# Optimization experiments

Hardware: AMD Instinct MI355X
Metric: run time of the kernel (lower is better)

## Reference

```python
import jax, jax.numpy as jnp
import numpy as np

N_NODES = 100000
N_EDGES = 1600000
IN_C = 64
HID = 64
OUT_C = 40


def setup_inputs() -> dict:
    key = jax.random.key(0)
    ks = jax.random.split(key, 12)
    def lin_init(k, fan_in, shape):
        bound = 1.0 / np.sqrt(fan_in)
        return jax.random.uniform(k, shape, jnp.float32, -bound, bound)
    x0 = jax.random.normal(ks[0], (N_NODES, IN_C), jnp.float32)
    edge_index = jax.random.randint(ks[1], (2, N_EDGES), 0, N_NODES, jnp.int64)
    return {
        "x0": x0,
        "edge_index": edge_index,
        "W1": lin_init(ks[2], IN_C, (HID, IN_C)),
        "b1": lin_init(ks[3], IN_C, (HID,)),
        "Wr1": lin_init(ks[4], IN_C, (HID, IN_C)),
        "br1": lin_init(ks[5], IN_C, (HID,)),
        "W2": lin_init(ks[6], HID, (HID, HID)),
        "b2": lin_init(ks[7], HID, (HID,)),
        "Wr2": lin_init(ks[8], HID, (HID, HID)),
        "br2": lin_init(ks[9], HID, (HID,)),
        "Wl": lin_init(ks[10], 2 * HID, (OUT_C, 2 * HID)),
        "bl": lin_init(ks[11], 2 * HID, (OUT_C,)),
    }


def _norm_weights(row, col, num_nodes):
    # symmetric degree normalization: d^-1/2[row] * d^-1/2[col]
    ones = jnp.ones(row.shape[0], jnp.float32)
    deg = jax.ops.segment_sum(ones, row, num_segments=num_nodes)
    dis = jnp.where(deg > 0, jax.lax.rsqrt(jnp.maximum(deg, 1.0)) * jnp.where(deg > 0, 1.0, 0.0), 0.0)
    dis = jnp.where(deg > 0, deg ** -0.5, 0.0)
    return dis[row] * dis[col]


def _bigraph_conv(x, row, col, w, W, b, Wr, br, num_nodes):
    h = x @ W.T + b                                    # [N, out]
    msg = w[:, None] * h[col]                          # gather + scale, [E, out]
    agg = jax.ops.segment_sum(msg, row, num_segments=num_nodes)
    return agg + x @ Wr.T + br


def reference(x0, edge_index, W1, b1, Wr1, br1, W2, b2, Wr2, br2, Wl, bl):
    num_nodes = x0.shape[0]
    row, col = edge_index[0], edge_index[1]
    w = _norm_weights(row, col, num_nodes)
    x1 = jax.nn.relu(_bigraph_conv(x0, row, col, w, W1, b1, Wr1, br1, num_nodes))
    x2 = jax.nn.relu(_bigraph_conv(x1, row, col, w, W2, b2, Wr2, br2, num_nodes))
    x = jnp.concatenate([x1, x2], axis=-1)
    logits = x @ Wl.T + bl
    return jax.nn.log_softmax(logits, axis=-1)
```

## Files before the change

kernel.cpp:

```cpp
#include <hip/hip_runtime.h>
#include <math.h>


typedef unsigned short u16;
typedef unsigned int   u32;

#define BROWS 512
#define BIN_CHUNK 8192
#define CAPB 12288

__device__ __forceinline__ u16 f2bf(float f) {
  u32 u = __float_as_uint(f);
  u32 r = u + 0x7fffu + ((u >> 16) & 1u);
  return (u16)(r >> 16);
}
__device__ __forceinline__ float bf2f(u16 h) {
  return __uint_as_float(((u32)h) << 16);
}

__global__ __launch_bounds__(1024) void k_binA(
    const int* __restrict__ row, const int* __restrict__ col,
    unsigned* __restrict__ bCnt, unsigned* __restrict__ pairs,
    int nE, int NB, int capA)
{
  __shared__ unsigned buf[BIN_CHUNK];
  __shared__ unsigned cnt[16][256];
  __shared__ unsigned base[256], gb[256], tot[256], sc[256];
  const int t = threadIdx.x;
  const int wave = t >> 6, lane = t & 63;
  const int tb = blockIdx.x * BIN_CHUNK;

  for (int i = t; i < 16 * 256; i += 1024) ((unsigned*)cnt)[i] = 0;
  __syncthreads();

  unsigned pk[8];
  unsigned short po[8];
  short bk[8];
#pragma unroll
  for (int j = 0; j < 8; ++j) {
    int i = tb + j * 1024 + t;
    if (i < nE) {
      int r = row[i], c = col[i];
      int b = r >> 9;
      pk[j] = ((unsigned)(r & (BROWS - 1)) << 17) | (unsigned)c;
      bk[j] = (short)b;
      po[j] = (unsigned short)atomicAdd(&cnt[wave][b], 1u);
    } else bk[j] = -1;
  }
  __syncthreads();

  if (t < 256) {
    unsigned run = 0;
#pragma unroll
    for (int w = 0; w < 16; ++w) {
      unsigned c = cnt[w][t];
      cnt[w][t] = run;
      run += c;
    }
    tot[t] = run;
    sc[t] = run;
  }
  __syncthreads();
  for (int off = 1; off < 256; off <<= 1) {
    unsigned v = 0;
    if (t < 256 && t >= off) v = sc[t - off];
    __syncthreads();
    if (t < 256) sc[t] += v;
    __syncthreads();
  }
  if (t < 256) {
    base[t] = t ? sc[t - 1] : 0u;
    unsigned c = tot[t];
    gb[t] = c ? atomicAdd(&bCnt[t], c) : 0u;
  }
  __syncthreads();

#pragma unroll
  for (int j = 0; j < 8; ++j)
    if (bk[j] >= 0) buf[base[bk[j]] + cnt[wave][bk[j]] + po[j]] = pk[j];
  __syncthreads();

  for (int b = wave; b < NB; b += 16) {
    unsigned cb = tot[b];
    if (!cb) continue;
    unsigned lo = base[b], g = gb[b];
    size_t dst = (size_t)b * (unsigned)capA;
    for (unsigned u = lane; u < cb; u += 64)
      if (g + u < (unsigned)capA) pairs[dst + g + u] = buf[lo + u];
  }
}

__global__ __launch_bounds__(256) void k_bscan(const unsigned* __restrict__ bCnt,
                                               unsigned* __restrict__ bBase, int NB) {
  __shared__ unsigned sc[256];
  int t = threadIdx.x;
  unsigned v = (t < NB) ? min(bCnt[t], (unsigned)CAPB) : 0u;
  sc[t] = v;
  __syncthreads();
  for (int off = 1; off < 256; off <<= 1) {
    unsigned u = (t >= off) ? sc[t - off] : 0u;
    __syncthreads();
    sc[t] += u;
    __syncthreads();
  }
  if (t < NB) bBase[t] = t ? sc[t - 1] : 0u;
}

__global__ __launch_bounds__(512) void k_binB(
    const unsigned* __restrict__ pairs, const unsigned* __restrict__ bCnt,
    const unsigned* __restrict__ bBase, int* __restrict__ colS,
    unsigned* __restrict__ start, float* __restrict__ dis,
    int N, int capA)
{
  __shared__ unsigned hist[BROWS], ex[BROWS], cur[BROWS], sc[BROWS];
  __shared__ unsigned cols[CAPB];
  const int t = threadIdx.x;
  const int b = blockIdx.x;
  const unsigned cnt = min(bCnt[b], (unsigned)CAPB);
  const unsigned gbase = bBase[b];
  const size_t src = (size_t)b * (unsigned)capA;

  hist[t] = 0;
  __syncthreads();
  for (unsigned i = t; i < cnt; i += 512)
    atomicAdd(&hist[pairs[src + i] >> 17], 1u);
  __syncthreads();
  const unsigned h = hist[t];
  sc[t] = h;
  __syncthreads();
  for (int off = 1; off < 512; off <<= 1) {
    unsigned v = (t >= off) ? sc[t - off] : 0u;
    __syncthreads();
    sc[t] += v;
    __syncthreads();
  }
  const unsigned e = sc[t] - h;
  ex[t] = e; cur[t] = e;
  __syncthreads();
  for (unsigned i = t; i < cnt; i += 512) {
    unsigned p = pairs[src + i];
    unsigned pos = atomicAdd(&cur[p >> 17], 1u);
    cols[pos] = p & 0x1FFFFu;
  }
  __syncthreads();
  for (unsigned i = t; i < cnt; i += 512)
    colS[gbase + i] = (int)cols[i];
  const int n = b * BROWS + t;
  if (n < N) {
    start[n] = gbase + e + h;
    dis[n] = h ? rsqrtf((float)h) : 0.f;
  }
}

__global__ __launch_bounds__(256) void k_deg(const int* __restrict__ row,
                                             unsigned* __restrict__ deg, int nE) {
  int i = blockIdx.x * blockDim.x + threadIdx.x;
  int stride = gridDim.x * blockDim.x;
  for (; i < nE; i += stride) atomicAdd(&deg[row[i]], 1u);
}

__global__ __launch_bounds__(256) void k_dis(const unsigned* __restrict__ deg,
                                             float* __restrict__ dis, int n) {
  int i = blockIdx.x * blockDim.x + threadIdx.x;
  if (i < n) {
    unsigned d = deg[i];
    dis[i] = d > 0u ? rsqrtf((float)d) : 0.f;
  }
}

__global__ __launch_bounds__(256) void k_scan1(const unsigned* __restrict__ deg,
                                               unsigned* __restrict__ start,
                                               unsigned* __restrict__ bsum, int n) {
  __shared__ unsigned s[256];
  const int base = blockIdx.x * 2048;
  unsigned v[8], tsum = 0;
#pragma unroll
  for (int j = 0; j < 8; ++j) {
    int idx = base + threadIdx.x * 8 + j;
    v[j] = idx < n ? deg[idx] : 0u;
    tsum += v[j];
  }
  s[threadIdx.x] = tsum;
  __syncthreads();
  for (int off = 1; off < 256; off <<= 1) {
    unsigned t = (threadIdx.x >= off) ? s[threadIdx.x - off] : 0u;
    __syncthreads();
    s[threadIdx.x] += t;
    __syncthreads();
  }
  unsigned run = threadIdx.x ? s[threadIdx.x - 1] : 0u;
  if (threadIdx.x == 255) bsum[blockIdx.x] = s[255];
#pragma unroll
  for (int j = 0; j < 8; ++j) {
    int idx = base + threadIdx.x * 8 + j;
    if (idx < n) start[idx] = run;
    run += v[j];
  }
}

__global__ void k_scan2(unsigned* __restrict__ bsum, int nB) {
  if (threadIdx.x == 0 && blockIdx.x == 0) {
    unsigned run = 0;
    for (int b = 0; b < nB; ++b) { unsigned t = bsum[b]; bsum[b] = run; run += t; }
  }
}

__global__ __launch_bounds__(256) void k_scan3(unsigned* __restrict__ start,
                                               const unsigned* __restrict__ bsum, int n) {
  int i = blockIdx.x * blockDim.x + threadIdx.x;
  if (i < n) start[i] += bsum[i >> 11];
}

__global__ __launch_bounds__(256) void k_build(const int* __restrict__ row,
                                               const int* __restrict__ col,
                                               unsigned* __restrict__ start,
                                               int* __restrict__ colS, int nE) {
  int i = blockIdx.x * blockDim.x + threadIdx.x;
  int stride = gridDim.x * blockDim.x;
  for (; i < nE; i += stride) {
    int r = row[i];
    unsigned p = atomicAdd(&start[r], 1u);
    colS[p] = col[i];
  }
}

__global__ __launch_bounds__(256) void k_cast(const float4* __restrict__ x4,
                                              ushort4* __restrict__ out, int n4) {
  int i = blockIdx.x * blockDim.x + threadIdx.x;
  int stride = gridDim.x * blockDim.x;
  for (; i < n4; i += stride) {
    float4 f = x4[i];
    ushort4 v;
    v.x = f2bf(f.x); v.y = f2bf(f.y); v.z = f2bf(f.z); v.w = f2bf(f.w);
    out[i] = v;
  }
}

__global__ __launch_bounds__(256) void k_prep(
    const float* __restrict__ W1, const float* __restrict__ b1,
    const float* __restrict__ Wr1, const float* __restrict__ br1,
    const float* __restrict__ W2, const float* __restrict__ b2,
    const float* __restrict__ Wr2, const float* __restrict__ br2,
    float4* __restrict__ UT)
{
  int i = blockIdx.x * 256 + threadIdx.x;
  if (i >= 2 * 33 * 64) return;
  int layer = i / (33 * 64);
  int kq = (i / 64) % 33;
  int o = i % 64;
  const float* W  = layer ? W2  : W1;
  const float* Wr = layer ? Wr2 : Wr1;
  const float* b  = layer ? b2  : b1;
  const float* br = layer ? br2 : br1;
  float4 v;
  if (kq < 16)       v = ((const float4*)W)[o * 16 + kq];
  else if (kq < 32)  v = ((const float4*)Wr)[o * 16 + kq - 16];
  else               v = make_float4(b[o], br[o], 0.f, 0.f);
  UT[i] = v;
}

__global__ __launch_bounds__(256) void k_spmm_h(
    const u16* __restrict__ xh, u16* __restrict__ aggh, float* __restrict__ rs,
    const int* __restrict__ colS, const unsigned* __restrict__ startEnd,
    const float* __restrict__ dis, int nNodes)
{
  const int t = threadIdx.x, wave = t >> 6, lane = t & 63;
  const int g = lane >> 4, sub = lane & 15;
  const int n = blockIdx.x * 4 + wave;
  if (n >= nNodes) return;
  const unsigned lo = n ? startEnd[n - 1] : 0u;
  const unsigned hi = startEnd[n];
  const ushort4* h4 = (const ushort4*)xh;
  float ax = 0.f, ay = 0.f, az = 0.f, aw = 0.f, sw = 0.f;
  for (unsigned base = lo; base < hi; base += 64) {
    const int cnt = (int)min(64u, hi - base);
    int   myc = (lane < cnt) ? colS[base + lane] : 0;
    float myw = (lane < cnt) ? dis[myc] : 0.f;
    sw += myw;
    for (int j = 0; j < cnt; j += 16) {
      int ja = j + g, jb = j + 4 + g, jc = j + 8 + g, jd = j + 12 + g;
      int   c0 = __shfl(myc, ja); float w0 = __shfl(myw, ja);
      int   c1 = __shfl(myc, jb); float w1 = __shfl(myw, jb);
      int   c2 = __shfl(myc, jc); float w2 = __shfl(myw, jc);
      int   c3 = __shfl(myc, jd); float w3 = __shfl(myw, jd);
      ushort4 v0 = h4[(size_t)c0 * 16 + sub];
      ushort4 v1 = h4[(size_t)c1 * 16 + sub];
      ushort4 v2 = h4[(size_t)c2 * 16 + sub];
      ushort4 v3 = h4[(size_t)c3 * 16 + sub];
      ax += w0 * bf2f(v0.x) + w1 * bf2f(v1.x) + w2 * bf2f(v2.x) + w3 * bf2f(v3.x);
      ay += w0 * bf2f(v0.y) + w1 * bf2f(v1.y) + w2 * bf2f(v2.y) + w3 * bf2f(v3.y);
      az += w0 * bf2f(v0.z) + w1 * bf2f(v1.z) + w2 * bf2f(v2.z) + w3 * bf2f(v3.z);
      aw += w0 * bf2f(v0.w) + w1 * bf2f(v1.w) + w2 * bf2f(v2.w) + w3 * bf2f(v3.w);
    }
  }
  ax += __shfl_xor(ax, 16); ay += __shfl_xor(ay, 16);
  az += __shfl_xor(az, 16); aw += __shfl_xor(aw, 16);
  ax += __shfl_xor(ax, 32); ay += __shfl_xor(ay, 32);
  az += __shfl_xor(az, 32); aw += __shfl_xor(aw, 32);
  sw += __shfl_xor(sw, 1);  sw += __shfl_xor(sw, 2);
  sw += __shfl_xor(sw, 4);  sw += __shfl_xor(sw, 8);
  sw += __shfl_xor(sw, 16); sw += __shfl_xor(sw, 32);
  const float dn = dis[n];
  if (lane < 16) {
    ushort4 o;
    o.x = f2bf(dn * ax); o.y = f2bf(dn * ay);
    o.z = f2bf(dn * az); o.w = f2bf(dn * aw);
    ((ushort4*)aggh)[(size_t)n * 16 + sub] = o;
  }
  if (lane == 0) rs[n] = dn * sw;
}

__global__ __launch_bounds__(256) void k_gemv(
    const u16* __restrict__ aggh, const float* __restrict__ rs,
    const u16* __restrict__ rooth, const float4* __restrict__ UT,
    u16* __restrict__ xo, int nNodes)
{
  __shared__ u16 xsh[64][136];
  const int t = threadIdx.x;
  const int lane = t & 63;
  const int og = __builtin_amdgcn_readfirstlane(t >> 6);
  const int n0 = blockIdx.x * 64;

  {
    const int r = t >> 2, q = t & 3;
    int gn = n0 + r; if (gn > nNodes - 1) gn = nNodes - 1;
    const uint4* a = (const uint4*)(aggh + (size_t)gn * 64);
    const uint4* x = (const uint4*)(rooth + (size_t)gn * 64);
    *(uint4*)&xsh[r][q * 16]           = a[q * 2];
    *(uint4*)&xsh[r][q * 16 + 8]       = a[q * 2 + 1];
    *(uint4*)&xsh[r][64 + q * 16]      = x[q * 2];
    *(uint4*)&xsh[r][64 + q * 16 + 8]  = x[q * 2 + 1];
  }
  __syncthreads();

  float acc[16];
#pragma unroll
  for (int j = 0; j < 16; ++j) acc[j] = 0.f;

#pragma unroll 4
  for (int k = 0; k < 32; ++k) {
    ushort4 v = *(const ushort4*)&xsh[lane][k * 4];
    float xa = bf2f(v.x), xb = bf2f(v.y), xc = bf2f(v.z), xd = bf2f(v.w);
    const float4* w = UT + k * 64 + og * 16;
#pragma unroll
    for (int j = 0; j < 16; ++j) {
      float4 W = w[j];
      acc[j] = fmaf(xa, W.x, fmaf(xb, W.y, fmaf(xc, W.z, fmaf(xd, W.w, acc[j]))));
    }
  }

  const int n = n0 + lane;
  const float rsv = (n < nNodes) ? rs[n] : 0.f;
  {
    const float4* w = UT + 32 * 64 + og * 16;
#pragma unroll
    for (int j = 0; j < 16; ++j) {
      float4 W = w[j];
      acc[j] = fmaf(rsv, W.x, acc[j]) + W.y;
    }
  }

  if (n < nNodes) {
    uint4 u0, u1;
    u0.x = (u32)f2bf(fmaxf(acc[0], 0.f))  | ((u32)f2bf(fmaxf(acc[1], 0.f)) << 16);
    u0.y = (u32)f2bf(fmaxf(acc[2], 0.f))  | ((u32)f2bf(fmaxf(acc[3], 0.f)) << 16);
    u0.z = (u32)f2bf(fmaxf(acc[4], 0.f))  | ((u32)f2bf(fmaxf(acc[5], 0.f)) << 16);
    u0.w = (u32)f2bf(fmaxf(acc[6], 0.f))  | ((u32)f2bf(fmaxf(acc[7], 0.f)) << 16);
    u1.x = (u32)f2bf(fmaxf(acc[8], 0.f))  | ((u32)f2bf(fmaxf(acc[9], 0.f)) << 16);
    u1.y = (u32)f2bf(fmaxf(acc[10], 0.f)) | ((u32)f2bf(fmaxf(acc[11], 0.f)) << 16);
    u1.z = (u32)f2bf(fmaxf(acc[12], 0.f)) | ((u32)f2bf(fmaxf(acc[13], 0.f)) << 16);
    u1.w = (u32)f2bf(fmaxf(acc[14], 0.f)) | ((u32)f2bf(fmaxf(acc[15], 0.f)) << 16);
    uint4* dst = (uint4*)(xo + (size_t)n * 64 + og * 16);
    dst[0] = u0;
    dst[1] = u1;
  }
}

__global__ __launch_bounds__(256) void k_final(
    const u16* __restrict__ x1h, const u16* __restrict__ x2h,
    const float* __restrict__ Wl, const float* __restrict__ bl,
    float* __restrict__ out, int nNodes)
{
  __shared__ float4 xs[64][33];
  __shared__ float redM[64][4];
  __shared__ float redS[64][4];
  const int t = threadIdx.x;
  const int lane = t & 63;
  const int og = __builtin_amdgcn_readfirstlane(t >> 6);
  const int nodeBase = blockIdx.x * 64;

  {
    const int sn = t >> 2, q = t & 3;
    int gn = nodeBase + sn;
    if (gn > nNodes - 1) gn = nNodes - 1;
    const ushort4* a = (q < 2) ? (const ushort4*)(x1h + (size_t)gn * 64)
                               : (const ushort4*)(x2h + (size_t)gn * 64);
    const int qq = q & 1;
#pragma unroll
    for (int j = 0; j < 8; ++j) {
      ushort4 v = a[qq * 8 + j];
      xs[sn][q * 8 + j] = make_float4(bf2f(v.x), bf2f(v.y), bf2f(v.z), bf2f(v.w));
    }
  }
  __syncthreads();

  const float4* W4 = (const float4*)Wl;
  float acc[10];
#pragma unroll
  for (int j = 0; j < 10; ++j) acc[j] = bl[og * 10 + j];
  for (int k = 0; k < 32; ++k) {
    float4 x = xs[lane][k];
#pragma unroll
    for (int j = 0; j < 10; ++j) {
      float4 w = W4[(og * 10 + j) * 32 + k];
      acc[j] += w.x * x.x + w.y * x.y + w.z * x.z + w.w * x.w;
    }
  }

  float m10 = acc[0];
#pragma unroll
  for (int j = 1; j < 10; ++j) m10 = fmaxf(m10, acc[j]);
  redM[lane][og] = m10;
  __syncthreads();
  float M = fmaxf(fmaxf(redM[lane][0], redM[lane][1]),
                  fmaxf(redM[lane][2], redM[lane][3]));
  float s10 = 0.f;
#pragma unroll
  for (int j = 0; j < 10; ++j) s10 += __expf(acc[j] - M);
  redS[lane][og] = s10;
  __syncthreads();
  const float S = redS[lane][0] + redS[lane][1] + redS[lane][2] + redS[lane][3];
  const float lse = M + __logf(S);

  const int n = nodeBase + lane;
  if (n < nNodes) {
    float2* o2 = (float2*)(out + (size_t)n * 40 + og * 10);
#pragma unroll
    for (int q = 0; q < 5; ++q)
      o2[q] = make_float2(acc[2 * q] - lse, acc[2 * q + 1] - lse);
  }
}

extern "C" void kernel_launch(void* const* d_in, const int* in_sizes, int n_in,
                              void* d_out, int out_size, void* d_ws, size_t ws_size,
                              hipStream_t stream) {
  const float* x0  = (const float*)d_in[0];
  const int*   ei  = (const int*)d_in[1];
  const float* W1  = (const float*)d_in[2];
  const float* b1  = (const float*)d_in[3];
  const float* Wr1 = (const float*)d_in[4];
  const float* br1 = (const float*)d_in[5];
  const float* W2  = (const float*)d_in[6];
  const float* b2  = (const float*)d_in[7];
  const float* Wr2 = (const float*)d_in[8];
  const float* br2 = (const float*)d_in[9];
  const float* Wl  = (const float*)d_in[10];
  const float* bl  = (const float*)d_in[11];
  float* out = (float*)d_out;

  const int N = in_sizes[0] / 64;
  const int E = in_sizes[1] / 2;
  const int* row = ei;
  const int* col = ei + E;

  const int NB = (N + BROWS - 1) / BROWS;
  const int capA = 16384;
  const int avg = E / (NB > 0 ? NB : 1);
  const bool binOK = (N <= 131072) && (NB <= 256) &&
                     (avg + 12 * (int)sqrtf((float)avg + 1.f) + 256 <= CAPB);

  size_t P = (size_t)NB * capA;
  if (P < (size_t)32 * N) P = (size_t)32 * N;

  const size_t UT_W = 2 * 33 * 64 * 4;
  const size_t needBin = 4 * (512 + P + (size_t)E + (size_t)3 * N + UT_W +
                              (size_t)32 * N + (size_t)32 * N);
  const size_t needCSR = 4 * ((size_t)4 * N + 64 + (size_t)E + UT_W +
                              (size_t)32 * N + (size_t)32 * N + (size_t)32 * N);

  unsigned *start = nullptr; float *dis = nullptr, *rsv = nullptr;
  int* colS = nullptr; float4* UT = nullptr;
  u16 *aggh = nullptr, *x0h = nullptr, *x1h = nullptr, *x2h = nullptr;
  bool ok = false;

  if (binOK && ws_size >= needBin) {
    unsigned* bCnt  = (unsigned*)d_ws;
    unsigned* bBase = bCnt + 256;
    unsigned* pairs = bBase + 256;
    colS  = (int*)(pairs + P);
    start = (unsigned*)(colS + E);
    dis   = (float*)(start + N);
    rsv   = dis + N;
    UT    = (float4*)(rsv + N);
    aggh  = (u16*)(UT + 2 * 33 * 64);
    x1h   = aggh + (size_t)64 * N;
    x0h   = (u16*)pairs;
    x2h   = (u16*)pairs;

    hipMemsetAsync(bCnt, 0, 256 * 4, stream);
    k_binA<<<(E + BIN_CHUNK - 1) / BIN_CHUNK, 1024, 0, stream>>>(row, col, bCnt, pairs, E, NB, capA);
    k_bscan<<<1, 256, 0, stream>>>(bCnt, bBase, NB);
    k_binB<<<NB, 512, 0, stream>>>(pairs, bCnt, bBase, colS, start, dis, N, capA);
    ok = true;
  } else if (ws_size >= needCSR) {
    unsigned* deg = (unsigned*)d_ws;
    start = deg + N;
    dis   = (float*)(start + N);
    rsv   = dis + N;
    unsigned* bsum = (unsigned*)(rsv + N);
    colS  = (int*)(bsum + 64);
    UT    = (float4*)(colS + E);
    aggh  = (u16*)(UT + 2 * 33 * 64);
    x1h   = aggh + (size_t)64 * N;
    u16* xsh = x1h + (size_t)64 * N;
    x0h = xsh; x2h = xsh;

    const int nB = (N + 2047) / 2048;
    hipMemsetAsync(deg, 0, (size_t)N * 4, stream);
    k_deg<<<1024, 256, 0, stream>>>(row, deg, E);
    k_dis<<<(N + 255) / 256, 256, 0, stream>>>(deg, dis, N);
    k_scan1<<<nB, 256, 0, stream>>>(deg, start, bsum, N);
    k_scan2<<<1, 64, 0, stream>>>(bsum, nB);
    k_scan3<<<(N + 255) / 256, 256, 0, stream>>>(start, bsum, N);
    k_build<<<1024, 256, 0, stream>>>(row, col, start, colS, E);
    ok = true;
  }

  if (!ok) return;

  k_cast<<<1024, 256, 0, stream>>>((const float4*)x0, (ushort4*)x0h, N * 16);
  k_prep<<<17, 256, 0, stream>>>(W1, b1, Wr1, br1, W2, b2, Wr2, br2, UT);

  k_spmm_h<<<(N + 3) / 4, 256, 0, stream>>>(x0h, aggh, rsv, colS, start, dis, N);
  k_gemv<<<(N + 63) / 64, 256, 0, stream>>>(aggh, rsv, x0h, UT, x1h, N);

  k_spmm_h<<<(N + 3) / 4, 256, 0, stream>>>(x1h, aggh, rsv, colS, start, dis, N);
  k_gemv<<<(N + 63) / 64, 256, 0, stream>>>(aggh, rsv, x1h, UT + 33 * 64, x2h, N);

  k_final<<<(N + 63) / 64, 256, 0, stream>>>(x1h, x2h, Wl, bl, out, N);
}
```

Before: 225.0 us.

## Precompute packed column/weight records and map one node per 16 lanes in SpMM

Adds a pass that builds per-edge (column, dis[col]) records and the row weight sums once, so both SpMM layers read packed records instead of gathering dis per edge and recomputing sums. The SpMM kernel now assigns 16 lanes per node instead of a whole 64-lane wave, removing shuffles and idle lanes for low-degree nodes. It costs an extra kernel and 8 bytes per edge of extra workspace traffic. Each node's lanes read its records serially.

```diff
diff --git a/kernel.cpp b/kernel.cpp
--- a/kernel.cpp
+++ b/kernel.cpp
@@ -112,7 +112,7 @@
     unsigned* __restrict__ start, float* __restrict__ dis,
     int N, int capA)
 {
-  __shared__ unsigned hist[BROWS], ex[BROWS], cur[BROWS], sc[BROWS];
+  __shared__ unsigned hist[BROWS], cur[BROWS], sc[BROWS];
   __shared__ unsigned cols[CAPB];
   const int t = threadIdx.x;
   const int b = blockIdx.x;
@@ -135,7 +135,7 @@
     __syncthreads();
   }
   const unsigned e = sc[t] - h;
-  ex[t] = e; cur[t] = e;
+  cur[t] = e;
   __syncthreads();
   for (unsigned i = t; i < cnt; i += 512) {
     unsigned p = pairs[src + i];
@@ -222,6 +222,29 @@
     unsigned p = atomicAdd(&start[r], 1u);
     colS[p] = col[i];
   }
+}
+
+__global__ __launch_bounds__(256) void k_wgt(
+    const int* __restrict__ colS, const unsigned* __restrict__ startEnd,
+    const float* __restrict__ dis, uint2* __restrict__ rec,
+    float* __restrict__ rs, int nNodes)
+{
+  const int t = threadIdx.x;
+  const int sub = t & 15;
+  const int n = blockIdx.x * 16 + (t >> 4);
+  if (n >= nNodes) return;
+  const unsigned lo = n ? startEnd[n - 1] : 0u;
+  const unsigned hi = startEnd[n];
+  float s = 0.f;
+  for (unsigned u = lo + sub; u < hi; u += 16) {
+    int c = colS[u];
+    float w = dis[c];
+    rec[u] = make_uint2((unsigned)c, __float_as_uint(w));
+    s += w;
+  }
+  s += __shfl_xor(s, 1); s += __shfl_xor(s, 2);
+  s += __shfl_xor(s, 4); s += __shfl_xor(s, 8);
+  if (sub == 0) rs[n] = dis[n] * s;
 }
 
 __global__ __launch_bounds__(256) void k_cast(const float4* __restrict__ x4,
@@ -259,55 +282,47 @@
   UT[i] = v;
 }
 
-__global__ __launch_bounds__(256) void k_spmm_h(
-    const u16* __restrict__ xh, u16* __restrict__ aggh, float* __restrict__ rs,
-    const int* __restrict__ colS, const unsigned* __restrict__ startEnd,
+__global__ __launch_bounds__(256) void k_spmm_rec(
+    const u16* __restrict__ xh, u16* __restrict__ aggh,
+    const uint2* __restrict__ rec, const unsigned* __restrict__ startEnd,
     const float* __restrict__ dis, int nNodes)
 {
-  const int t = threadIdx.x, wave = t >> 6, lane = t & 63;
-  const int g = lane >> 4, sub = lane & 15;
-  const int n = blockIdx.x * 4 + wave;
+  const int t = threadIdx.x;
+  const int sub = t & 15;
+  const int n = blockIdx.x * 16 + (t >> 4);
   if (n >= nNodes) return;
   const unsigned lo = n ? startEnd[n - 1] : 0u;
   const unsigned hi = startEnd[n];
   const ushort4* h4 = (const ushort4*)xh;
-  float ax = 0.f, ay = 0.f, az = 0.f, aw = 0.f, sw = 0.f;
-  for (unsigned base = lo; base < hi; base += 64) {
-    const int cnt = (int)min(64u, hi - base);
-    int   myc = (lane < cnt) ? colS[base + lane] : 0;
-    float myw = (lane < cnt) ? dis[myc] : 0.f;
-    sw += myw;
-    for (int j = 0; j < cnt; j += 16) {
-      int ja = j + g, jb = j + 4 + g, jc = j + 8 + g, jd = j + 12 + g;
-      int   c0 = __shfl(myc, ja); float w0 = __shfl(myw, ja);
-      int   c1 = __shfl(myc, jb); float w1 = __shfl(myw, jb);
-      int   c2 = __shfl(myc, jc); float w2 = __shfl(myw, jc);
-      int   c3 = __shfl(myc, jd); float w3 = __shfl(myw, jd);
-      ushort4 v0 = h4[(size_t)c0 * 16 + sub];
-      ushort4 v1 = h4[(size_t)c1 * 16 + sub];
-      ushort4 v2 = h4[(size_t)c2 * 16 + sub];
-      ushort4 v3 = h4[(size_t)c3 * 16 + sub];
-      ax += w0 * bf2f(v0.x) + w1 * bf2f(v1.x) + w2 * bf2f(v2.x) + w3 * bf2f(v3.x);
-      ay += w0 * bf2f(v0.y) + w1 * bf2f(v1.y) + w2 * bf2f(v2.y) + w3 * bf2f(v3.y);
-      az += w0 * bf2f(v0.z) + w1 * bf2f(v1.z) + w2 * bf2f(v2.z) + w3 * bf2f(v3.z);
-      aw += w0 * bf2f(v0.w) + w1 * bf2f(v1.w) + w2 * bf2f(v2.w) + w3 * bf2f(v3.w);
-    }
-  }
-  ax += __shfl_xor(ax, 16); ay += __shfl_xor(ay, 16);
-  az += __shfl_xor(az, 16); aw += __shfl_xor(aw, 16);
-  ax += __shfl_xor(ax, 32); ay += __shfl_xor(ay, 32);
-  az += __shfl_xor(az, 32); aw += __shfl_xor(aw, 32);
-  sw += __shfl_xor(sw, 1);  sw += __shfl_xor(sw, 2);
-  sw += __shfl_xor(sw, 4);  sw += __shfl_xor(sw, 8);
-  sw += __shfl_xor(sw, 16); sw += __shfl_xor(sw, 32);
+
+  float ax = 0.f, ay = 0.f, az = 0.f, aw = 0.f;
+  unsigned p = lo;
+  for (; p + 4 <= hi; p += 4) {
+    uint2 r0 = rec[p],     r1 = rec[p + 1];
+    uint2 r2 = rec[p + 2], r3 = rec[p + 3];
+    ushort4 v0 = h4[(size_t)r0.x * 16 + sub];
+    ushort4 v1 = h4[(size_t)r1.x * 16 + sub];
+    ushort4 v2 = h4[(size_t)r2.x * 16 + sub];
+    ushort4 v3 = h4[(size_t)r3.x * 16 + sub];
+    float w0 = __uint_as_float(r0.y), w1 = __uint_as_float(r1.y);
+    float w2 = __uint_as_float(r2.y), w3 = __uint_as_float(r3.y);
+    ax += w0 * bf2f(v0.x) + w1 * bf2f(v1.x) + w2 * bf2f(v2.x) + w3 * bf2f(v3.x);
+    ay += w0 * bf2f(v0.y) + w1 * bf2f(v1.y) + w2 * bf2f(v2.y) + w3 * bf2f(v3.y);
+    az += w0 * bf2f(v0.z) + w1 * bf2f(v1.z) + w2 * bf2f(v2.z) + w3 * bf2f(v3.z);
+    aw += w0 * bf2f(v0.w) + w1 * bf2f(v1.w) + w2 * bf2f(v2.w) + w3 * bf2f(v3.w);
+  }
+  for (; p < hi; ++p) {
+    uint2 r = rec[p];
+    ushort4 v = h4[(size_t)r.x * 16 + sub];
+    float w = __uint_as_float(r.y);
+    ax += w * bf2f(v.x); ay += w * bf2f(v.y);
+    az += w * bf2f(v.z); aw += w * bf2f(v.w);
+  }
   const float dn = dis[n];
-  if (lane < 16) {
-    ushort4 o;
-    o.x = f2bf(dn * ax); o.y = f2bf(dn * ay);
-    o.z = f2bf(dn * az); o.w = f2bf(dn * aw);
-    ((ushort4*)aggh)[(size_t)n * 16 + sub] = o;
-  }
-  if (lane == 0) rs[n] = dn * sw;
+  ushort4 o;
+  o.x = f2bf(dn * ax); o.y = f2bf(dn * ay);
+  o.z = f2bf(dn * az); o.w = f2bf(dn * aw);
+  ((ushort4*)aggh)[(size_t)n * 16 + sub] = o;
 }
 
 __global__ __launch_bounds__(256) void k_gemv(
@@ -473,13 +488,13 @@
   if (P < (size_t)32 * N) P = (size_t)32 * N;
 
   const size_t UT_W = 2 * 33 * 64 * 4;
-  const size_t needBin = 4 * (512 + P + (size_t)E + (size_t)3 * N + UT_W +
+  const size_t needBin = 4 * (512 + P + (size_t)3 * E + (size_t)3 * N + UT_W +
                               (size_t)32 * N + (size_t)32 * N);
-  const size_t needCSR = 4 * ((size_t)4 * N + 64 + (size_t)E + UT_W +
+  const size_t needCSR = 4 * ((size_t)4 * N + 64 + (size_t)3 * E + UT_W +
                               (size_t)32 * N + (size_t)32 * N + (size_t)32 * N);
 
   unsigned *start = nullptr; float *dis = nullptr, *rsv = nullptr;
-  int* colS = nullptr; float4* UT = nullptr;
+  int* colS = nullptr; uint2* rec = nullptr; float4* UT = nullptr;
   u16 *aggh = nullptr, *x0h = nullptr, *x1h = nullptr, *x2h = nullptr;
   bool ok = false;
 
@@ -488,7 +503,8 @@
     unsigned* bBase = bCnt + 256;
     unsigned* pairs = bBase + 256;
     colS  = (int*)(pairs + P);
-    start = (unsigned*)(colS + E);
+    rec   = (uint2*)(colS + E);
+    start = (unsigned*)(rec + E);
     dis   = (float*)(start + N);
     rsv   = dis + N;
     UT    = (float4*)(rsv + N);
@@ -509,7 +525,8 @@
     rsv   = dis + N;
     unsigned* bsum = (unsigned*)(rsv + N);
     colS  = (int*)(bsum + 64);
-    UT    = (float4*)(colS + E);
+    rec   = (uint2*)(colS + E);
+    UT    = (float4*)(rec + E);
     aggh  = (u16*)(UT + 2 * 33 * 64);
     x1h   = aggh + (size_t)64 * N;
     u16* xsh = x1h + (size_t)64 * N;
@@ -528,13 +545,14 @@
 
   if (!ok) return;
 
+  k_wgt<<<(N + 15) / 16, 256, 0, stream>>>(colS, start, dis, rec, rsv, N);
   k_cast<<<1024, 256, 0, stream>>>((const float4*)x0, (ushort4*)x0h, N * 16);
   k_prep<<<17, 256, 0, stream>>>(W1, b1, Wr1, br1, W2, b2, Wr2, br2, UT);
 
-  k_spmm_h<<<(N + 3) / 4, 256, 0, stream>>>(x0h, aggh, rsv, colS, start, dis, N);
+  k_spmm_rec<<<(N + 15) / 16, 256, 0, stream>>>(x0h, aggh, rec, start, dis, N);
   k_gemv<<<(N + 63) / 64, 256, 0, stream>>>(aggh, rsv, x0h, UT, x1h, N);
 
-  k_spmm_h<<<(N + 3) / 4, 256, 0, stream>>>(x1h, aggh, rsv, colS, start, dis, N);
+  k_spmm_rec<<<(N + 15) / 16, 256, 0, stream>>>(x1h, aggh, rec, start, dis, N);
   k_gemv<<<(N + 63) / 64, 256, 0, stream>>>(aggh, rsv, x1h, UT + 33 * 64, x2h, N);
 
   k_final<<<(N + 63) / 64, 256, 0, stream>>>(x1h, x2h, Wl, bl, out, N);
```

Result: no change. 225.1 us, median of 2 (+0.0%).
